# Optimization experiments

Hardware: AMD Instinct MI355X
Metric: run time of the kernel (lower is better)

The kernel has to match this reference:

```python
import jax, jax.numpy as jnp
import numpy as np

N = 100000      # num nodes
E = 3200000     # num edges
R = 8           # num relations
C_IN, HID, C_OUT = 128, 64, 64


def rgcn_conv(x, W, root, bias, src, dst, etype):
    """One RGCNConv layer (PyG semantics, mean aggregation per relation).
    out[i] = bias + x[i] @ root + sum_r mean_{j in N_r(i)} x[j] @ W[r]
    """
    n = x.shape[0]
    # transform-then-gather: [R, N, H] avoids per-edge [E, C, H] matmuls
    xW = jnp.einsum('nc,rch->rnh', x, W)
    msg = xW[etype, src]                              # [E, H]
    # per-(relation, target-node) in-degree for mean normalization
    seg = etype * n + dst
    deg = jax.ops.segment_sum(jnp.ones((src.shape[0],), dtype=x.dtype), seg,
                              num_segments=R * n)      # [R*N]
    msg = msg / jnp.maximum(deg[seg], 1.0)[:, None]
    agg = jax.ops.segment_sum(msg, dst, num_segments=n)  # [N, H]
    return agg + x @ root + bias


def setup_inputs() -> dict:
    key = jax.random.key(0)
    ks = jax.random.split(key, 9)
    x = jax.random.normal(ks[0], (N, C_IN), dtype=jnp.float32)
    edge_index = jax.random.randint(ks[1], (2, E), 0, N)
    edge_type = jax.random.randint(ks[2], (E,), 0, R)
    s1 = 1.0 / np.sqrt(C_IN)
    s2 = 1.0 / np.sqrt(HID)
    W1 = jax.random.normal(ks[3], (R, C_IN, HID), dtype=jnp.float32) * s1
    root1 = jax.random.normal(ks[4], (C_IN, HID), dtype=jnp.float32) * s1
    b1 = jnp.zeros((HID,), dtype=jnp.float32)
    W2 = jax.random.normal(ks[5], (R, HID, C_OUT), dtype=jnp.float32) * s2
    root2 = jax.random.normal(ks[6], (HID, C_OUT), dtype=jnp.float32) * s2
    b2 = jnp.zeros((C_OUT,), dtype=jnp.float32)
    return {"x": x, "edge_index": edge_index, "edge_type": edge_type,
            "W1": W1, "root1": root1, "b1": b1,
            "W2": W2, "root2": root2, "b2": b2}


def reference(x, edge_index, edge_type, W1, root1, b1, W2, root2, b2):
    src, dst = edge_index[0], edge_index[1]
    h = rgcn_conv(x, W1, root1, b1, src, dst, edge_type)
    h = jax.nn.relu(h)  # dropout p=0.0 is identity
    out = rgcn_conv(h, W2, root2, b2, src, dst, edge_type)
    return out
```

## Files before the change

kernel.cpp:

```cpp
#include <hip/hip_runtime.h>

#define N_NODES 100000
#define N_EDGES 3200000
#define R_REL   8
#define C_IN    128
#define HID     64
#define WCOLS   576

#define NBUCK 500
#define NPB   200
#define NBLK  256
#define CHUNK 12500
#define NCELL (NBUCK * NBLK)
#define BCAP  7680

typedef __attribute__((ext_vector_type(8))) short  short8;
typedef __attribute__((ext_vector_type(4))) float  float4v;

__device__ __forceinline__ float bf2f(unsigned short u) {
    union { unsigned int i; float f; } v; v.i = ((unsigned int)u) << 16; return v.f;
}
__device__ __forceinline__ unsigned short f2bf(float f) {
    union { float f; unsigned int i; } v; v.f = f;
    unsigned int r = v.i + 0x7FFFu + ((v.i >> 16) & 1u);
    return (unsigned short)(r >> 16);
}
__device__ __forceinline__ float rl_f(float v, int j) {
    union { float f; int i; } a, b; a.f = v;
    b.i = __builtin_amdgcn_readlane(a.i, j);
    return b.f;
}

__global__ void prep_wcat(const float* __restrict__ W1,
                          const float* __restrict__ root1,
                          const float* __restrict__ W2,
                          const float* __restrict__ root2,
                          unsigned short* __restrict__ BT1,
                          unsigned short* __restrict__ BT2) {
    int idx = blockIdx.x * 256 + threadIdx.x;
    const int T1 = WCOLS * C_IN;
    const int T2 = WCOLS * HID;
    if (idx < T1) {
        int c = idx / C_IN, k = idx % C_IN;
        float v;
        if (c < 512) { int r = c >> 6, h = c & 63; v = W1[r * (C_IN * 64) + k * 64 + h]; }
        else         { v = root1[k * 64 + (c - 512)]; }
        BT1[idx] = f2bf(v);
    } else if (idx < T1 + T2) {
        int j = idx - T1;
        int c = j / HID, k = j % HID;
        float v;
        if (c < 512) { int r = c >> 6, h = c & 63; v = W2[r * (HID * 64) + k * 64 + h]; }
        else         { v = root2[k * 64 + (c - 512)]; }
        BT2[j] = f2bf(v);
    }
}

__global__ __launch_bounds__(1024)
void edge_sort_local(const int* __restrict__ src, const int* __restrict__ dst,
                     const int* __restrict__ et,
                     unsigned int* __restrict__ esort,
                     int* __restrict__ bcountT, int* __restrict__ lstartT) {
    __shared__ int cnt[NBUCK], cur[NBUCK], tsum[1024];
    __shared__ unsigned int sedge[CHUNK];
    const int blk = blockIdx.x, tid = threadIdx.x;
    const int e0 = blk * CHUNK;

    for (int i = tid; i < NBUCK; i += 1024) cnt[i] = 0;
    __syncthreads();
    for (int i = tid; i < CHUNK; i += 1024)
        atomicAdd(&cnt[dst[e0 + i] / NPB], 1);
    __syncthreads();

    int v = (tid < NBUCK) ? cnt[tid] : 0;
    tsum[tid] = v; __syncthreads();
    for (int off = 1; off < 1024; off <<= 1) {
        int t = (tid >= off) ? tsum[tid - off] : 0;
        __syncthreads(); tsum[tid] += t; __syncthreads();
    }
    if (tid < NBUCK) cur[tid] = tsum[tid] - v;
    __syncthreads();

    for (int b = tid; b < NBUCK; b += 1024) {
        bcountT[blk * NBUCK + b] = cnt[b];
        lstartT[blk * NBUCK + b] = cur[b];
    }
    __syncthreads();

    for (int i = tid; i < CHUNK; i += 1024) {
        int d = dst[e0 + i];
        int b = d / NPB;
        int pos = atomicAdd(&cur[b], 1);
        sedge[pos] = ((unsigned int)src[e0 + i] << 11) |
                     ((unsigned int)(d - b * NPB) << 3) | (unsigned int)et[e0 + i];
    }
    __syncthreads();
    for (int i = tid; i < CHUNK; i += 1024) esort[e0 + i] = sedge[i];
}

__global__ __launch_bounds__(1024)
void bucket_build(const unsigned int* __restrict__ esort,
                  const int* __restrict__ bcountT, const int* __restrict__ lstartT,
                  unsigned int* __restrict__ elist,
                  int* __restrict__ rowstart8) {
    __shared__ int   cnt[2048], cur[2048], tsum[1024];
    __shared__ int   rpos[NBLK], rloff[NBLK];
    __shared__ unsigned int sedge[BCAP];
    __shared__ unsigned int selist[BCAP];

    const int b = blockIdx.x, tid = threadIdx.x;

    for (int i = tid; i < 2048; i += 1024) cnt[i] = 0;
    int myrl = 0, myls = 0;
    if (tid < NBLK) {
        myrl = bcountT[tid * NBUCK + b];
        myls = lstartT[tid * NBUCK + b];
        rpos[tid] = tid * CHUNK + myls;
    }
    __syncthreads();

    tsum[tid] = myrl; __syncthreads();
    for (int off = 1; off < 1024; off <<= 1) {
        int t = (tid >= off) ? tsum[tid - off] : 0;
        __syncthreads(); tsum[tid] += t; __syncthreads();
    }
    const int total = tsum[NBLK - 1];
    if (tid < NBLK) rloff[tid] = tsum[tid] - myrl;
    __syncthreads();

    tsum[tid] = myls; __syncthreads();
    for (int off = 512; off > 0; off >>= 1) {
        if (tid < off) tsum[tid] += tsum[tid + off];
        __syncthreads();
    }
    const int seg0 = tsum[0];
    __syncthreads();
    const bool fits = (total <= BCAP);

    for (int i = tid; i < total; i += 1024) {
        int lo = 0, hi = NBLK - 1;
        while (lo < hi) { int mid = (lo + hi + 1) >> 1; if (rloff[mid] <= i) lo = mid; else hi = mid - 1; }
        unsigned int e = esort[rpos[lo] + (i - rloff[lo])];
        if (fits) sedge[i] = e;
        atomicAdd(&cnt[(int)((e >> 3) & 255u) * 8 + (int)(e & 7u)], 1);
    }
    __syncthreads();

    int base = tid * 2;
    int c0 = cnt[base], c1 = cnt[base + 1];
    int s = c0 + c1;
    tsum[tid] = s; __syncthreads();
    for (int off = 1; off < 1024; off <<= 1) {
        int t = (tid >= off) ? tsum[tid - off] : 0;
        __syncthreads(); tsum[tid] += t; __syncthreads();
    }
    int texcl = tsum[tid] - s;
    cur[base] = texcl; cur[base + 1] = texcl + c0;
    __syncthreads();

    for (int i = tid; i < NPB * 8; i += 1024)
        rowstart8[(b * NPB) * 8 + i] = seg0 + cur[i];
    if (b == NBUCK - 1 && tid == 0) rowstart8[N_NODES * 8] = N_EDGES;
    __syncthreads();

    for (int i = tid; i < total; i += 1024) {
        unsigned int e;
        if (fits) e = sedge[i];
        else {
            int lo = 0, hi = NBLK - 1;
            while (lo < hi) { int mid = (lo + hi + 1) >> 1; if (rloff[mid] <= i) lo = mid; else hi = mid - 1; }
            e = esort[rpos[lo] + (i - rloff[lo])];
        }
        int r = (int)(e & 7u);
        int j = (int)((e >> 3) & 255u) * 8 + r;
        int p = atomicAdd(&cur[j], 1);
        unsigned int eo = (e >> 11) * WCOLS + (unsigned int)(r * 64);
        if (fits) selist[p] = eo;
        else      elist[seg0 + p] = eo;
    }
    __syncthreads();

    if (fits) {
        for (int i = tid; i < total; i += 1024)
            elist[seg0 + i] = selist[i];
    }
}

template <int K, bool AF32>
__global__ __launch_bounds__(256)
void gemm_rows(const void* __restrict__ Araw,
               const unsigned short* __restrict__ BT,
               unsigned short* __restrict__ Out, int nrows) {
    constexpr int KSTEPS = K / 32;
    constexpr int LDB = K + 8;
    __shared__ __align__(16) unsigned short Blds[64 * LDB];
    __shared__ __align__(16) unsigned short stage[4][16 * 64];

    const int wave = threadIdx.x >> 6;
    const int lane = threadIdx.x & 63;
    const int l15 = lane & 15, quad = lane >> 4;
    const int rowbase = blockIdx.x * 64 + wave * 16;
    int arow = rowbase + l15;
    if (arow >= nrows) arow = nrows - 1;

    short8 afrag[KSTEPS];
    if constexpr (AF32) {
        const float* Af = (const float*)Araw;
#pragma unroll
        for (int ks = 0; ks < KSTEPS; ++ks) {
            const float* p = Af + (size_t)arow * K + ks * 32 + quad * 8;
            float4v u0 = *(const float4v*)p;
            float4v u1 = *(const float4v*)(p + 4);
            short8 f;
            f[0] = (short)f2bf(u0[0]); f[1] = (short)f2bf(u0[1]);
            f[2] = (short)f2bf(u0[2]); f[3] = (short)f2bf(u0[3]);
            f[4] = (short)f2bf(u1[0]); f[5] = (short)f2bf(u1[1]);
            f[6] = (short)f2bf(u1[2]); f[7] = (short)f2bf(u1[3]);
            afrag[ks] = f;
        }
    } else {
        const unsigned short* Ab = (const unsigned short*)Araw;
#pragma unroll
        for (int ks = 0; ks < KSTEPS; ++ks)
            afrag[ks] = *(const short8*)(Ab + (size_t)arow * K + ks * 32 + quad * 8);
    }

    for (int chunk = 0; chunk < 9; ++chunk) {
        __syncthreads();
        {
            const unsigned short* src = BT + (size_t)chunk * 64 * K;
            const int nvec = 64 * K / 8;
            for (int i = threadIdx.x; i < nvec; i += 256) {
                int r = i / (K / 8);
                int cpos = (i % (K / 8)) * 8;
                *(uint4*)(&Blds[r * LDB + cpos]) = *(const uint4*)(src + r * K + cpos);
            }
        }
        __syncthreads();

        float4v acc[4];
#pragma unroll
        for (int ct = 0; ct < 4; ++ct) { acc[ct][0] = 0.f; acc[ct][1] = 0.f; acc[ct][2] = 0.f; acc[ct][3] = 0.f; }

#pragma unroll
        for (int ct = 0; ct < 4; ++ct) {
#pragma unroll
            for (int ks = 0; ks < KSTEPS; ++ks) {
                short8 bfrag = *(const short8*)(&Blds[(ct * 16 + l15) * LDB + ks * 32 + quad * 8]);
                acc[ct] = __builtin_amdgcn_mfma_f32_16x16x32_bf16(afrag[ks], bfrag, acc[ct], 0, 0, 0);
            }
        }

#pragma unroll
        for (int ct = 0; ct < 4; ++ct)
#pragma unroll
            for (int r = 0; r < 4; ++r)
                stage[wave][(quad * 4 + r) * 64 + ct * 16 + l15] = f2bf(acc[ct][r]);
        __syncthreads();

        {
            int r = lane >> 2, j = lane & 3;
            int orow = rowbase + r;
            if (orow < nrows) {
#pragma unroll
                for (int p = 0; p < 2; ++p) {
                    int c0 = (j + p * 4) * 8;
                    uint4 v = *(const uint4*)&stage[wave][r * 64 + c0];
                    *(uint4*)(Out + (size_t)orow * WCOLS + chunk * 64 + c0) = v;
                }
            }
        }
    }
}

template <int MODE>
__global__ __launch_bounds__(256)
void agg_fused(const unsigned short* __restrict__ XW,
               const unsigned int* __restrict__ elist,
               const int* __restrict__ rowstart8,
               const float* __restrict__ bias,
               void* __restrict__ outp) {
    const int wave = threadIdx.x >> 6, lane = threadIdx.x & 63;
    const int n = blockIdx.x * 4 + wave;
    int r9 = 0;
    if (lane < 9) r9 = rowstart8[n * 8 + lane];
    const int b0 = __builtin_amdgcn_readlane(r9, 0);
    const int b1 = __builtin_amdgcn_readlane(r9, 1);
    const int b2 = __builtin_amdgcn_readlane(r9, 2);
    const int b3 = __builtin_amdgcn_readlane(r9, 3);
    const int b4 = __builtin_amdgcn_readlane(r9, 4);
    const int b5 = __builtin_amdgcn_readlane(r9, 5);
    const int b6 = __builtin_amdgcn_readlane(r9, 6);
    const int b7 = __builtin_amdgcn_readlane(r9, 7);
    const int b8 = __builtin_amdgcn_readlane(r9, 8);
    const int beg = b0, end = b8;

    auto invlen = [](int a, int bnd) {
        int l = bnd - a; return 1.0f / (float)(l > 1 ? l : 1);
    };
    const float il0 = invlen(b0, b1), il1 = invlen(b1, b2);
    const float il2 = invlen(b2, b3), il3 = invlen(b3, b4);
    const float il4 = invlen(b4, b5), il5 = invlen(b5, b6);
    const float il6 = invlen(b6, b7), il7 = invlen(b7, b8);

    const unsigned short* XWl = XW + lane;

    float acc = 0.f;
    int i = beg;
    while (i < end) {
        int m = end - i; if (m > 64) m = 64;
        int idx = i + lane; if (idx >= end) idx = end - 1;
        unsigned int ub = elist[idx];
        float wb = il0;
        wb = (idx >= b1) ? il1 : wb;
        wb = (idx >= b2) ? il2 : wb;
        wb = (idx >= b3) ? il3 : wb;
        wb = (idx >= b4) ? il4 : wb;
        wb = (idx >= b5) ? il5 : wb;
        wb = (idx >= b6) ? il6 : wb;
        wb = (idx >= b7) ? il7 : wb;

        int j = 0;
        for (; j + 16 <= m; j += 16) {
            float vv[16], ww[16];
#pragma unroll
            for (int t = 0; t < 16; ++t) {
                unsigned int u = (unsigned int)__builtin_amdgcn_readlane((int)ub, j + t);
                ww[t] = rl_f(wb, j + t);
                vv[t] = bf2f(XWl[u]);
            }
#pragma unroll
            for (int t = 0; t < 16; ++t) acc += ww[t] * vv[t];
        }
        for (; j + 4 <= m; j += 4) {
            float vv[4], ww[4];
#pragma unroll
            for (int t = 0; t < 4; ++t) {
                unsigned int u = (unsigned int)__builtin_amdgcn_readlane((int)ub, j + t);
                ww[t] = rl_f(wb, j + t);
                vv[t] = bf2f(XWl[u]);
            }
#pragma unroll
            for (int t = 0; t < 4; ++t) acc += ww[t] * vv[t];
        }
        for (; j < m; ++j) {
            unsigned int u = (unsigned int)__builtin_amdgcn_readlane((int)ub, j);
            float w = rl_f(wb, j);
            acc += w * bf2f(XWl[u]);
        }
        i += m;
    }

    float res = acc + bf2f(XW[(size_t)n * WCOLS + 512 + lane]) + bias[lane];
    if (MODE == 0) {
        res = res > 0.f ? res : 0.f;
        ((unsigned short*)outp)[(size_t)n * 64 + lane] = f2bf(res);
    } else {
        ((float*)outp)[(size_t)n * 64 + lane] = res;
    }
}

extern "C" void kernel_launch(void* const* d_in, const int* in_sizes, int n_in,
                              void* d_out, int out_size, void* d_ws, size_t ws_size,
                              hipStream_t stream) {
    const float* x     = (const float*)d_in[0];
    const int*   eidx  = (const int*)d_in[1];
    const int*   etyp  = (const int*)d_in[2];
    const float* W1    = (const float*)d_in[3];
    const float* root1 = (const float*)d_in[4];
    const float* b1    = (const float*)d_in[5];
    const float* W2    = (const float*)d_in[6];
    const float* root2 = (const float*)d_in[7];
    const float* b2    = (const float*)d_in[8];
    float*       out   = (float*)d_out;

    char* ws = (char*)d_ws;
    size_t off = 0;
    auto alloc = [&](size_t bytes) { char* p = ws + off; off += (bytes + 255) & ~(size_t)255; return p; };

    unsigned short* xW       = (unsigned short*)alloc((size_t)N_NODES * WCOLS * 2);
    unsigned short* h        = (unsigned short*)alloc((size_t)N_NODES * HID * 2);
    unsigned int*   elist    = (unsigned int*)alloc((size_t)N_EDGES * 4);
    int*            rowstart8= (int*)alloc(((size_t)N_NODES * 8 + 1) * 4);
    unsigned short* BT1      = (unsigned short*)alloc((size_t)WCOLS * C_IN * 2);
    unsigned short* BT2      = (unsigned short*)alloc((size_t)WCOLS * HID * 2);

    unsigned int* esort   = (unsigned int*)xW;
    int*          bcountT = (int*)((char*)xW + (size_t)N_EDGES * 4);
    int*          lstartT = bcountT + NCELL;

    const int* srcp = eidx;
    const int* dstp = eidx + N_EDGES;

    prep_wcat<<<(WCOLS * (C_IN + HID) + 255) / 256, 256, 0, stream>>>(W1, root1, W2, root2, BT1, BT2);

    edge_sort_local<<<NBLK, 1024, 0, stream>>>(srcp, dstp, etyp, esort, bcountT, lstartT);
    bucket_build<<<NBUCK, 1024, 0, stream>>>(esort, bcountT, lstartT, elist, rowstart8);

    const int gemm_grid = (N_NODES + 63) / 64;
    const int agg_grid  = N_NODES / 4;

    gemm_rows<C_IN, true><<<gemm_grid, 256, 0, stream>>>((const void*)x, BT1, xW, N_NODES);
    agg_fused<0><<<agg_grid, 256, 0, stream>>>(xW, elist, rowstart8, b1, (void*)h);

    gemm_rows<HID, false><<<gemm_grid, 256, 0, stream>>>((const void*)h, BT2, xW, N_NODES);
    agg_fused<1><<<agg_grid, 256, 0, stream>>>(xW, elist, rowstart8, b2, (void*)out);
}
```

Before: 380.6 us.

## Double-buffer B tiles in layer-1 GEMM and make layer-2 GEMM persistent

The generic gemm_rows kernel is split into two specialised kernels. Layer 1 now uses 512-thread blocks covering 128 rows, and it double-buffers each 64-column B chunk in LDS, prefetching the next chunk into registers during the MFMAs so each chunk needs one barrier instead of two. Layer 2 loads the whole 576x64 B matrix into LDS once per block and runs a persistent grid of 256 blocks that loop over row tiles, which removes the repeated B reloads and barriers. The trade-off is higher LDS use per block, which can reduce occupancy, and a fixed grid size that may not balance across all CUs.

```diff
diff --git a/kernel.cpp b/kernel.cpp
--- a/kernel.cpp
+++ b/kernel.cpp
@@ -186,78 +186,67 @@
     }
 }
 
-template <int K, bool AF32>
-__global__ __launch_bounds__(256)
-void gemm_rows(const void* __restrict__ Araw,
-               const unsigned short* __restrict__ BT,
-               unsigned short* __restrict__ Out, int nrows) {
-    constexpr int KSTEPS = K / 32;
+__global__ __launch_bounds__(512)
+void gemm_l1(const float* __restrict__ A,
+             const unsigned short* __restrict__ BT,
+             unsigned short* __restrict__ Out, int nrows) {
+    constexpr int K = C_IN;
     constexpr int LDB = K + 8;
-    __shared__ __align__(16) unsigned short Blds[64 * LDB];
-    __shared__ __align__(16) unsigned short stage[4][16 * 64];
-
-    const int wave = threadIdx.x >> 6;
-    const int lane = threadIdx.x & 63;
+    __shared__ __align__(16) unsigned short Blds[2][64 * LDB];
+    __shared__ __align__(16) unsigned short stage[8][16 * 64];
+
+    const int wave = threadIdx.x >> 6, lane = threadIdx.x & 63;
     const int l15 = lane & 15, quad = lane >> 4;
-    const int rowbase = blockIdx.x * 64 + wave * 16;
+    const int rowbase = blockIdx.x * 128 + wave * 16;
     int arow = rowbase + l15;
     if (arow >= nrows) arow = nrows - 1;
 
-    short8 afrag[KSTEPS];
-    if constexpr (AF32) {
-        const float* Af = (const float*)Araw;
-#pragma unroll
-        for (int ks = 0; ks < KSTEPS; ++ks) {
-            const float* p = Af + (size_t)arow * K + ks * 32 + quad * 8;
-            float4v u0 = *(const float4v*)p;
-            float4v u1 = *(const float4v*)(p + 4);
-            short8 f;
-            f[0] = (short)f2bf(u0[0]); f[1] = (short)f2bf(u0[1]);
-            f[2] = (short)f2bf(u0[2]); f[3] = (short)f2bf(u0[3]);
-            f[4] = (short)f2bf(u1[0]); f[5] = (short)f2bf(u1[1]);
-            f[6] = (short)f2bf(u1[2]); f[7] = (short)f2bf(u1[3]);
-            afrag[ks] = f;
-        }
-    } else {
-        const unsigned short* Ab = (const unsigned short*)Araw;
-#pragma unroll
-        for (int ks = 0; ks < KSTEPS; ++ks)
-            afrag[ks] = *(const short8*)(Ab + (size_t)arow * K + ks * 32 + quad * 8);
-    }
-
+    short8 afrag[4];
+#pragma unroll
+    for (int ks = 0; ks < 4; ++ks) {
+        const float* p = A + (size_t)arow * K + ks * 32 + quad * 8;
+        float4v u0 = *(const float4v*)p;
+        float4v u1 = *(const float4v*)(p + 4);
+        short8 f;
+        f[0] = (short)f2bf(u0[0]); f[1] = (short)f2bf(u0[1]);
+        f[2] = (short)f2bf(u0[2]); f[3] = (short)f2bf(u0[3]);
+        f[4] = (short)f2bf(u1[0]); f[5] = (short)f2bf(u1[1]);
+        f[6] = (short)f2bf(u1[2]); f[7] = (short)f2bf(u1[3]);
+        afrag[ks] = f;
+    }
+
+    for (int i = threadIdx.x; i < 1024; i += 512) {
+        int r = i >> 4, c = (i & 15) * 8;
+        *(uint4*)&Blds[0][r * LDB + c] = *(const uint4*)(BT + r * K + c);
+    }
+    __syncthreads();
+
+    int cur = 0;
     for (int chunk = 0; chunk < 9; ++chunk) {
-        __syncthreads();
-        {
-            const unsigned short* src = BT + (size_t)chunk * 64 * K;
-            const int nvec = 64 * K / 8;
-            for (int i = threadIdx.x; i < nvec; i += 256) {
-                int r = i / (K / 8);
-                int cpos = (i % (K / 8)) * 8;
-                *(uint4*)(&Blds[r * LDB + cpos]) = *(const uint4*)(src + r * K + cpos);
-            }
-        }
-        __syncthreads();
+        uint4 p0, p1;
+        const int i0 = threadIdx.x, i1 = threadIdx.x + 512;
+        if (chunk < 8) {
+            const unsigned short* src = BT + (size_t)(chunk + 1) * 64 * K;
+            p0 = *(const uint4*)(src + (i0 >> 4) * K + (i0 & 15) * 8);
+            p1 = *(const uint4*)(src + (i1 >> 4) * K + (i1 & 15) * 8);
+        }
 
         float4v acc[4];
 #pragma unroll
         for (int ct = 0; ct < 4; ++ct) { acc[ct][0] = 0.f; acc[ct][1] = 0.f; acc[ct][2] = 0.f; acc[ct][3] = 0.f; }
-
-#pragma unroll
-        for (int ct = 0; ct < 4; ++ct) {
-#pragma unroll
-            for (int ks = 0; ks < KSTEPS; ++ks) {
-                short8 bfrag = *(const short8*)(&Blds[(ct * 16 + l15) * LDB + ks * 32 + quad * 8]);
+#pragma unroll
+        for (int ct = 0; ct < 4; ++ct)
+#pragma unroll
+            for (int ks = 0; ks < 4; ++ks) {
+                short8 bfrag = *(const short8*)(&Blds[cur][(ct * 16 + l15) * LDB + ks * 32 + quad * 8]);
                 acc[ct] = __builtin_amdgcn_mfma_f32_16x16x32_bf16(afrag[ks], bfrag, acc[ct], 0, 0, 0);
             }
-        }
 
 #pragma unroll
         for (int ct = 0; ct < 4; ++ct)
 #pragma unroll
             for (int r = 0; r < 4; ++r)
                 stage[wave][(quad * 4 + r) * 64 + ct * 16 + l15] = f2bf(acc[ct][r]);
-        __syncthreads();
-
         {
             int r = lane >> 2, j = lane & 3;
             int orow = rowbase + r;
@@ -267,6 +256,74 @@
                     int c0 = (j + p * 4) * 8;
                     uint4 v = *(const uint4*)&stage[wave][r * 64 + c0];
                     *(uint4*)(Out + (size_t)orow * WCOLS + chunk * 64 + c0) = v;
+                }
+            }
+        }
+
+        if (chunk < 8) {
+            *(uint4*)&Blds[cur ^ 1][(i0 >> 4) * LDB + (i0 & 15) * 8] = p0;
+            *(uint4*)&Blds[cur ^ 1][(i1 >> 4) * LDB + (i1 & 15) * 8] = p1;
+            cur ^= 1;
+        }
+        __syncthreads();
+    }
+}
+
+__global__ __launch_bounds__(512)
+void gemm_l2(const unsigned short* __restrict__ A,
+             const unsigned short* __restrict__ BT,
+             unsigned short* __restrict__ Out, int nrows) {
+    constexpr int K = HID;
+    constexpr int LDB = K + 8;
+    __shared__ __align__(16) unsigned short Blds[WCOLS * LDB];
+    __shared__ __align__(16) unsigned short stage[8][16 * 64];
+
+    const int wave = threadIdx.x >> 6, lane = threadIdx.x & 63;
+    const int l15 = lane & 15, quad = lane >> 4;
+
+    for (int i = threadIdx.x; i < WCOLS * K / 8; i += 512) {
+        int c = i >> 3, kv = (i & 7) * 8;
+        *(uint4*)&Blds[c * LDB + kv] = *(const uint4*)(BT + c * K + kv);
+    }
+    __syncthreads();
+
+    const int ntiles = (nrows + 127) / 128;
+    for (int t = blockIdx.x; t < ntiles; t += gridDim.x) {
+        const int rowbase = t * 128 + wave * 16;
+        int arow = rowbase + l15;
+        if (arow >= nrows) arow = nrows - 1;
+        short8 afrag[2];
+#pragma unroll
+        for (int ks = 0; ks < 2; ++ks)
+            afrag[ks] = *(const short8*)(A + (size_t)arow * K + ks * 32 + quad * 8);
+
+        for (int chunk = 0; chunk < 9; ++chunk) {
+            float4v acc[4];
+#pragma unroll
+            for (int ct = 0; ct < 4; ++ct) { acc[ct][0] = 0.f; acc[ct][1] = 0.f; acc[ct][2] = 0.f; acc[ct][3] = 0.f; }
+#pragma unroll
+            for (int ct = 0; ct < 4; ++ct)
+#pragma unroll
+                for (int ks = 0; ks < 2; ++ks) {
+                    short8 bfrag = *(const short8*)(&Blds[(chunk * 64 + ct * 16 + l15) * LDB + ks * 32 + quad * 8]);
+                    acc[ct] = __builtin_amdgcn_mfma_f32_16x16x32_bf16(afrag[ks], bfrag, acc[ct], 0, 0, 0);
+                }
+
+#pragma unroll
+            for (int ct = 0; ct < 4; ++ct)
+#pragma unroll
+                for (int r = 0; r < 4; ++r)
+                    stage[wave][(quad * 4 + r) * 64 + ct * 16 + l15] = f2bf(acc[ct][r]);
+            {
+                int r = lane >> 2, j = lane & 3;
+                int orow = rowbase + r;
+                if (orow < nrows) {
+#pragma unroll
+                    for (int p = 0; p < 2; ++p) {
+                        int c0 = (j + p * 4) * 8;
+                        uint4 v = *(const uint4*)&stage[wave][r * 64 + c0];
+                        *(uint4*)(Out + (size_t)orow * WCOLS + chunk * 64 + c0) = v;
+                    }
                 }
             }
         }
@@ -397,12 +454,12 @@
     edge_sort_local<<<NBLK, 1024, 0, stream>>>(srcp, dstp, etyp, esort, bcountT, lstartT);
     bucket_build<<<NBUCK, 1024, 0, stream>>>(esort, bcountT, lstartT, elist, rowstart8);
 
-    const int gemm_grid = (N_NODES + 63) / 64;
-    const int agg_grid  = N_NODES / 4;
-
-    gemm_rows<C_IN, true><<<gemm_grid, 256, 0, stream>>>((const void*)x, BT1, xW, N_NODES);
+    const int gemm1_grid = (N_NODES + 127) / 128;
+    const int agg_grid   = N_NODES / 4;
+
+    gemm_l1<<<gemm1_grid, 512, 0, stream>>>(x, BT1, xW, N_NODES);
     agg_fused<0><<<agg_grid, 256, 0, stream>>>(xW, elist, rowstart8, b1, (void*)h);
 
-    gemm_rows<HID, false><<<gemm_grid, 256, 0, stream>>>((const void*)h, BT2, xW, N_NODES);
+    gemm_l2<<<256, 512, 0, stream>>>(h, BT2, xW, N_NODES);
     agg_fused<1><<<agg_grid, 256, 0, stream>>>(xW, elist, rowstart8, b2, (void*)out);
 }
```

Result: no change. 379.0 us (-0.4%).
